# Kernel optimization log

Measured on AMD Instinct MI355X. Metric: run time of the kernel, lower is better.

## Reference

```python
import jax, jax.numpy as jnp
import numpy as np

NIN = 1024
NOUT = 1024
NHEADS = 16
DHEAD = NOUT // NHEADS


def setup_inputs() -> dict:
    key = jax.random.key(0)
    k1, k2, k3, k4 = jax.random.split(key, 4)
    y = jax.random.normal(k1, (2, 2048, NIN), dtype=jnp.float32)
    Wqkv = jax.random.normal(k2, (NIN, 3 * NOUT), dtype=jnp.float32) * (1.0 / np.sqrt(NIN))
    Wff = jax.random.normal(k3, (NOUT, NOUT), dtype=jnp.float32) * (1.0 / np.sqrt(NOUT))
    bff = jax.random.normal(k4, (NOUT,), dtype=jnp.float32) * 0.01
    return {"y": y, "Wqkv": Wqkv, "Wff": Wff, "bff": bff}


def reference(y, Wqkv, Wff, bff):
    b, n, _ = y.shape
    qkv = y @ Wqkv  # [b, n, 3*nout]
    qkv = qkv.reshape(b, n, 3, NHEADS, DHEAD).transpose(2, 0, 3, 1, 4)
    q, k, v = qkv[0], qkv[1], qkv[2]  # each [b, h, n, d]
    att = jnp.einsum('bhqd,bhkd->bhqk', q, k)
    causal = jnp.triu(jnp.ones((n, n), dtype=bool), k=1)
    att = jnp.where(causal, -jnp.inf, att)
    att = jax.nn.softmax(att / jnp.sqrt(jnp.float32(DHEAD)), axis=-1)
    ctx = jnp.einsum('bhqk,bhkd->bhqd', att, v)
    ctx = ctx.transpose(0, 2, 1, 3).reshape(b, n, NOUT)
    return ctx @ Wff + bff
```

## Files before the change

kernel.cpp:

```cpp
#include <hip/hip_runtime.h>
#include <stdint.h>

#define NHEADS 16
#define DHEAD 64
#define SEQ 2048
#define BATCH 2
#define NINF 1024
#define NOUTF 1024
#define N3 3072
#define MTOT 4096

typedef unsigned short US;
typedef __attribute__((ext_vector_type(8))) short short8;
typedef __attribute__((ext_vector_type(4))) short short4v;
typedef __attribute__((ext_vector_type(4))) float f32x4;

__device__ inline US f2bf(float f) {
  union { float f; unsigned u; } v; v.f = f;
  unsigned r = v.u + 0x7fffu + ((v.u >> 16) & 1u);
  return (US)(r >> 16);
}

__device__ inline f32x4 mfma16(short8 a, short8 b, f32x4 c) {
  return __builtin_amdgcn_mfma_f32_16x16x32_bf16(a, b, c, 0, 0, 0);
}

__device__ inline f32x4 mfma16k16(short4v a, short4v b, f32x4 c) {
  return __builtin_amdgcn_mfma_f32_16x16x16bf16_1k(a, b, c, 0, 0, 0);
}

__device__ inline void async16(const US* g, US* l) {
  __builtin_amdgcn_global_load_lds(
      (const __attribute__((address_space(1))) unsigned int*)g,
      (__attribute__((address_space(3))) unsigned int*)l, 16, 0, 0);
}

__global__ void k_convert(const float* __restrict__ src, US* __restrict__ dst, int n4) {
  int i = blockIdx.x * blockDim.x + threadIdx.x;
  if (i >= n4) return;
  float4 v = ((const float4*)src)[i];
  ushort4 o;
  o.x = f2bf(v.x); o.y = f2bf(v.y); o.z = f2bf(v.z); o.w = f2bf(v.w);
  ((ushort4*)dst)[i] = o;
}

__global__ void k_wtrans(const float* __restrict__ Wqkv, const float* __restrict__ Wff,
                         US* __restrict__ dq, US* __restrict__ df) {
  __shared__ float tile[32][33];
  int bxi = blockIdx.x;
  const float* src; US* dst; int C;
  if (bxi < 96) { src = Wqkv; dst = dq; C = N3; }
  else          { src = Wff;  dst = df; C = NOUTF; bxi -= 96; }
  int bx = bxi * 32, by = blockIdx.y * 32;
  int tx = threadIdx.x, ty = threadIdx.y;
  for (int i = 0; i < 32; i += 8)
    tile[ty + i][tx] = src[(size_t)(by + ty + i) * C + bx + tx];
  __syncthreads();
  for (int i = 0; i < 32; i += 8)
    dst[(size_t)(bx + ty + i) * 1024 + by + tx] = f2bf(tile[tx][ty + i]);
}

__global__ __launch_bounds__(256) void k_gemm_qkv(
    const US* __restrict__ A,
    const US* __restrict__ Bt,
    US* __restrict__ qbuf, US* __restrict__ kbuf, US* __restrict__ vtbuf) {
  __shared__ US As[128 * 32];
  __shared__ US Bs[128 * 32];
  int tid = threadIdx.x;
  int wave = tid >> 6, lane = tid & 63, lm = lane & 15, lk = lane >> 4;
  int wm = wave >> 1, wn = wave & 1;
  int mbase = blockIdx.y * 128, nbase = blockIdx.x * 128;
  int which = nbase >> 10;

  f32x4 acc[4][4];
#pragma unroll
  for (int i = 0; i < 4; ++i)
#pragma unroll
    for (int j = 0; j < 4; ++j) acc[i][j] = (f32x4){0.f, 0.f, 0.f, 0.f};

  const US* ga = A + (size_t)(mbase + (tid >> 2)) * NINF + (tid & 3) * 8;
  const US* gb = Bt + (size_t)(nbase + (tid >> 2)) * NINF + (tid & 3) * 8;
  US* la = As + tid * 8;
  US* lb = Bs + tid * 8;

  for (int kt = 0; kt < NINF / 32; ++kt) {
    int ko = kt * 32;
    async16(ga + ko, la);
    async16(ga + ko + (size_t)64 * NINF, la + 64 * 32);
    async16(gb + ko, lb);
    async16(gb + ko + (size_t)64 * NINF, lb + 64 * 32);
    __syncthreads();
    short8 a[4], b[4];
#pragma unroll
    for (int i = 0; i < 4; ++i)
      a[i] = *(const short8*)(As + (wm * 64 + i * 16 + lm) * 32 + lk * 8);
#pragma unroll
    for (int j = 0; j < 4; ++j)
      b[j] = *(const short8*)(Bs + (wn * 64 + j * 16 + lm) * 32 + lk * 8);
    if (which != 2) {
#pragma unroll
      for (int i = 0; i < 4; ++i)
#pragma unroll
        for (int j = 0; j < 4; ++j) acc[i][j] = mfma16(b[j], a[i], acc[i][j]);
    } else {
#pragma unroll
      for (int i = 0; i < 4; ++i)
#pragma unroll
        for (int j = 0; j < 4; ++j) acc[i][j] = mfma16(a[i], b[j], acc[i][j]);
    }
    __syncthreads();
  }

  int hh = ((nbase + wn * 64) & 1023) >> 6;
  if (which != 2) {
    US* dsts = (which == 0) ? qbuf : kbuf;
    float sc = (which == 0) ? 0.18033688011112042f : 1.f;
#pragma unroll
    for (int i = 0; i < 4; ++i) {
      int row = mbase + wm * 64 + i * 16 + lm;
      int bh = (row >> 11) * NHEADS + hh;
      int s = row & (SEQ - 1);
      US* base = dsts + ((size_t)bh * SEQ + s) * DHEAD;
#pragma unroll
      for (int j = 0; j < 4; ++j) {
        int d0 = j * 16 + lk * 4;
        uint32_t lo = (uint32_t)f2bf(acc[i][j][0] * sc) | ((uint32_t)f2bf(acc[i][j][1] * sc) << 16);
        uint32_t hi = (uint32_t)f2bf(acc[i][j][2] * sc) | ((uint32_t)f2bf(acc[i][j][3] * sc) << 16);
        uint2 pv; pv.x = lo; pv.y = hi;
        *(uint2*)(base + d0) = pv;
      }
    }
  } else {
#pragma unroll
    for (int j = 0; j < 4; ++j) {
      int d = j * 16 + lm;
#pragma unroll
      for (int i = 0; i < 4; ++i) {
        int row0 = mbase + wm * 64 + i * 16 + lk * 4;
        int bh = (row0 >> 11) * NHEADS + hh;
        int s0 = row0 & (SEQ - 1);
        uint32_t lo = (uint32_t)f2bf(acc[i][j][0]) | ((uint32_t)f2bf(acc[i][j][1]) << 16);
        uint32_t hi = (uint32_t)f2bf(acc[i][j][2]) | ((uint32_t)f2bf(acc[i][j][3]) << 16);
        uint2 pv; pv.x = lo; pv.y = hi;
        *(uint2*)(vtbuf + ((size_t)bh * DHEAD + d) * SEQ + s0) = pv;
      }
    }
  }
}

__global__ __launch_bounds__(256) void k_attn(
    const US* __restrict__ qbuf, const US* __restrict__ kbuf,
    const US* __restrict__ vtbuf, US* __restrict__ ctx) {
  __shared__ US Ks[2][64 * 64];
  __shared__ US Vs[2][64 * 64];
  int tid = threadIdx.x;
  int w = tid >> 6, lane = tid & 63;
  int lm = lane & 15, lk = lane >> 4;
  int bl = blockIdx.x;
  int xcd = bl & 7, g = bl >> 3;
  int bh = (g & 3) * 8 + xcd;
  int q4 = g >> 2;
  int rnd = q4 >> 3, qq = q4 & 7;
  int s = (rnd == 0) ? 31 - qq : (rnd == 1) ? qq : (rnd == 2) ? 23 - qq : 8 + qq;
  int qb = s * 64 + w * 16;
  int nt = s + 1;

  const US* kbase = kbuf + (size_t)bh * SEQ * DHEAD;
  const US* vtb = vtbuf + (size_t)bh * DHEAD * SEQ;
  const US* qr = qbuf + ((size_t)bh * SEQ + qb + lm) * DHEAD + lk * 8;
  short8 qf0 = *(const short8*)(qr);
  short8 qf1 = *(const short8*)(qr + 32);

  int swz = ((lane & 7) ^ (lane >> 3)) * 8;
  const US* gsrc[4];
  US* ldst[4];
  int step[4];
#pragma unroll
  for (int j = 0; j < 4; ++j) {
    int u = w + 4 * j;
    if (u < 8) {
      gsrc[j] = kbase + (size_t)(u * 8 + (lane >> 3)) * DHEAD + swz;
      ldst[j] = &Ks[0][0] + u * 512 + lane * 8;
      step[j] = 64 * DHEAD;
    } else {
      int i = u - 8;
      gsrc[j] = vtb + (size_t)(i * 8 + (lane >> 3)) * SEQ + swz;
      ldst[j] = &Vs[0][0] + i * 512 + lane * 8;
      step[j] = 64;
    }
  }

  int xorv = lm & 7;
  int ck0 = ((lk) ^ xorv) * 16;
  int ck1 = ((4 + lk) ^ xorv) * 16;
  int cv[4];
#pragma unroll
  for (int kg = 0; kg < 4; ++kg)
    cv[kg] = (((kg * 2 + (lk >> 1)) ^ xorv) * 16) + (lk & 1) * 8;

  f32x4 o[4];
#pragma unroll
  for (int dg = 0; dg < 4; ++dg) o[dg] = (f32x4){0.f, 0.f, 0.f, 0.f};
  f32x4 lacc = (f32x4){0.f, 0.f, 0.f, 0.f};
  const short4v kones = {(short)0x3F80, (short)0x3F80, (short)0x3F80, (short)0x3F80};

  auto body = [&](const char* Kc, const char* Vc, int kg, bool dm) {
    const char* kr = Kc + (kg * 16 + lm) * 128;
    short8 ka0 = *(const short8*)(kr + ck0);
    short8 ka1 = *(const short8*)(kr + ck1);
    f32x4 st = (f32x4){0.f, 0.f, 0.f, 0.f};
    st = mfma16(ka0, qf0, st);
    st = mfma16(ka1, qf1, st);
    uint32_t ue[4];
#pragma unroll
    for (int r = 0; r < 4; ++r) {
      float v = st[r];
      if (dm && (lk * 4 + r > lm)) v = -INFINITY;
      union { float f; uint32_t u; } cv2;
      cv2.f = exp2f(v);
      ue[r] = cv2.u + 0x8000u;
    }
    union { short4v s4; uint32_t u[2]; } pk;
    pk.u[0] = __builtin_amdgcn_perm(ue[1], ue[0], 0x07060302u);
    pk.u[1] = __builtin_amdgcn_perm(ue[3], ue[2], 0x07060302u);
    lacc = mfma16k16(kones, pk.s4, lacc);
    const char* vr = Vc + lm * 128 + cv[kg];
#pragma unroll
    for (int dg = 0; dg < 4; ++dg) {
      short4v va = *(const short4v*)(vr + dg * 2048);
      o[dg] = mfma16k16(va, pk.s4, o[dg]);
    }
  };

#pragma unroll
  for (int j = 0; j < 4; ++j) { async16(gsrc[j], ldst[j]); gsrc[j] += step[j]; }
  if (nt > 1) {
#pragma unroll
    for (int j = 0; j < 4; ++j) { async16(gsrc[j], ldst[j] + 4096); gsrc[j] += step[j]; }
  }

  for (int t = 0; t < nt; ++t) {
    if (t + 1 < nt) asm volatile("s_waitcnt vmcnt(4)" ::: "memory");
    else            asm volatile("s_waitcnt vmcnt(0)" ::: "memory");
    __builtin_amdgcn_s_barrier();
    asm volatile("" ::: "memory");
    const char* Kc = (const char*)Ks + (t & 1) * 8192;
    const char* Vc = (const char*)Vs + (t & 1) * 8192;
    if (t < s) {
#pragma unroll
      for (int kg = 0; kg < 4; ++kg) body(Kc, Vc, kg, false);
    } else {
      for (int kg = 0; kg < w; ++kg) body(Kc, Vc, kg, false);
      body(Kc, Vc, w, true);
    }
    asm volatile("" ::: "memory");
    __builtin_amdgcn_s_barrier();
    asm volatile("" ::: "memory");
    if (t + 2 < nt) {
#pragma unroll
      for (int j = 0; j < 4; ++j) {
        async16(gsrc[j], ldst[j] + (t & 1) * 4096);
        gsrc[j] += step[j];
      }
    }
  }

  float inv = 1.f / lacc[0];

  US* crow = ctx + ((size_t)(bh >> 4) * SEQ + qb + lm) * NOUTF + (bh & 15) * DHEAD;
#pragma unroll
  for (int dg = 0; dg < 4; ++dg) {
    union { short4v s4; uint32_t u[2]; } pk;
    pk.u[0] = (uint32_t)f2bf(o[dg][0] * inv) | ((uint32_t)f2bf(o[dg][1] * inv) << 16);
    pk.u[1] = (uint32_t)f2bf(o[dg][2] * inv) | ((uint32_t)f2bf(o[dg][3] * inv) << 16);
    *(short4v*)(crow + dg * 16 + lk * 4) = pk.s4;
  }
}

__global__ __launch_bounds__(256) void k_gemm_out(
    const US* __restrict__ A, const US* __restrict__ Bt,
    const float* __restrict__ bias, float* __restrict__ out) {
  __shared__ US As[128 * 32];
  __shared__ US Bs[64 * 32];
  int tid = threadIdx.x;
  int wave = tid >> 6, lane = tid & 63, lm = lane & 15, lk = lane >> 4;
  int mbase = blockIdx.y * 128, nbase = blockIdx.x * 64;

  f32x4 acc[2][4];
#pragma unroll
  for (int i = 0; i < 2; ++i)
#pragma unroll
    for (int j = 0; j < 4; ++j) acc[i][j] = (f32x4){0.f, 0.f, 0.f, 0.f};

  const US* ga = A + (size_t)(mbase + (tid >> 2)) * NOUTF + (tid & 3) * 8;
  const US* gb = Bt + (size_t)(nbase + (tid >> 2)) * NOUTF + (tid & 3) * 8;
  US* la = As + tid * 8;
  US* lb = Bs + tid * 8;

  for (int kt = 0; kt < NOUTF / 32; ++kt) {
    int ko = kt * 32;
    async16(ga + ko, la);
    async16(ga + ko + (size_t)64 * NOUTF, la + 64 * 32);
    async16(gb + ko, lb);
    __syncthreads();
    short8 a[2], b[4];
#pragma unroll
    for (int i = 0; i < 2; ++i)
      a[i] = *(const short8*)(As + (wave * 32 + i * 16 + lm) * 32 + lk * 8);
#pragma unroll
    for (int j = 0; j < 4; ++j)
      b[j] = *(const short8*)(Bs + (j * 16 + lm) * 32 + lk * 8);
#pragma unroll
    for (int i = 0; i < 2; ++i)
#pragma unroll
      for (int j = 0; j < 4; ++j) acc[i][j] = mfma16(b[j], a[i], acc[i][j]);
    __syncthreads();
  }

#pragma unroll
  for (int j = 0; j < 4; ++j) {
    int n0 = nbase + j * 16 + lk * 4;
    float4 bv = *(const float4*)(bias + n0);
#pragma unroll
    for (int i = 0; i < 2; ++i) {
      int row = mbase + wave * 32 + i * 16 + lm;
      float4 ov;
      ov.x = acc[i][j][0] + bv.x;
      ov.y = acc[i][j][1] + bv.y;
      ov.z = acc[i][j][2] + bv.z;
      ov.w = acc[i][j][3] + bv.w;
      *(float4*)(out + (size_t)row * NOUTF + n0) = ov;
    }
  }
}

extern "C" void kernel_launch(void* const* d_in, const int* in_sizes, int n_in,
                              void* d_out, int out_size, void* d_ws, size_t ws_size,
                              hipStream_t stream) {
  const float* y    = (const float*)d_in[0];
  const float* Wqkv = (const float*)d_in[1];
  const float* Wff  = (const float*)d_in[2];
  const float* bff  = (const float*)d_in[3];
  float* out = (float*)d_out;

  char* ws = (char*)d_ws;
  US* ybf   = (US*)(ws);
  US* ctx   = (US*)(ws);
  US* wqkvt = (US*)(ws + (8u << 20));
  US* wfft  = (US*)(ws + (14u << 20));
  US* qbuf  = (US*)(ws + (16u << 20));
  US* kbuf  = (US*)(ws + (24u << 20));
  US* vtbuf = (US*)(ws + (40u << 20));

  k_convert<<<MTOT * NINF / 4 / 256, 256, 0, stream>>>(y, ybf, MTOT * NINF / 4);
  k_wtrans<<<dim3(128, 32), dim3(32, 8), 0, stream>>>(Wqkv, Wff, wqkvt, wfft);
  k_gemm_qkv<<<dim3(N3 / 128, MTOT / 128), 256, 0, stream>>>(ybf, wqkvt, qbuf, kbuf, vtbuf);
  k_attn<<<dim3(1024), 256, 0, stream>>>(qbuf, kbuf, vtbuf, ctx);
  k_gemm_out<<<dim3(NOUTF / 64, MTOT / 128), 256, 0, stream>>>(ctx, wfft, bff, out);
}
```

Baseline: 192.9 us.

## Double-buffer LDS tiles in QKV and output GEMMs with async prefetch

Both projection GEMMs now keep two LDS buffers and prefetch the k-tile two steps ahead with async global-to-LDS loads. Explicit vmcnt waits and raw barriers replace the per-iteration __syncthreads. The goal is to overlap global memory latency with MFMA work instead of stalling each k-step. This doubles LDS use per block, which may lower occupancy, and depends on the hand-counted vmcnt values matching the number of outstanding loads.

```diff
diff --git a/kernel.cpp b/kernel.cpp
--- a/kernel.cpp
+++ b/kernel.cpp
@@ -64,8 +64,8 @@
     const US* __restrict__ A,
     const US* __restrict__ Bt,
     US* __restrict__ qbuf, US* __restrict__ kbuf, US* __restrict__ vtbuf) {
-  __shared__ US As[128 * 32];
-  __shared__ US Bs[128 * 32];
+  __shared__ US As[2][128 * 32];
+  __shared__ US Bs[2][128 * 32];
   int tid = threadIdx.x;
   int wave = tid >> 6, lane = tid & 63, lm = lane & 15, lk = lane >> 4;
   int wm = wave >> 1, wn = wave & 1;
@@ -80,35 +80,70 @@
 
   const US* ga = A + (size_t)(mbase + (tid >> 2)) * NINF + (tid & 3) * 8;
   const US* gb = Bt + (size_t)(nbase + (tid >> 2)) * NINF + (tid & 3) * 8;
-  US* la = As + tid * 8;
-  US* lb = Bs + tid * 8;
-
-  for (int kt = 0; kt < NINF / 32; ++kt) {
+  US* la = &As[0][0] + tid * 8;
+  US* lb = &Bs[0][0] + tid * 8;
+
+  auto STAGE = [&](int kt, int buf) {
     int ko = kt * 32;
-    async16(ga + ko, la);
-    async16(ga + ko + (size_t)64 * NINF, la + 64 * 32);
-    async16(gb + ko, lb);
-    async16(gb + ko + (size_t)64 * NINF, lb + 64 * 32);
-    __syncthreads();
-    short8 a[4], b[4];
-#pragma unroll
-    for (int i = 0; i < 4; ++i)
-      a[i] = *(const short8*)(As + (wm * 64 + i * 16 + lm) * 32 + lk * 8);
-#pragma unroll
-    for (int j = 0; j < 4; ++j)
-      b[j] = *(const short8*)(Bs + (wn * 64 + j * 16 + lm) * 32 + lk * 8);
-    if (which != 2) {
+    async16(ga + ko, la + buf * 4096);
+    async16(ga + ko + (size_t)64 * NINF, la + buf * 4096 + 2048);
+    async16(gb + ko, lb + buf * 4096);
+    async16(gb + ko + (size_t)64 * NINF, lb + buf * 4096 + 2048);
+  };
+
+  STAGE(0, 0);
+  STAGE(1, 1);
+
+  if (which != 2) {
+    for (int t = 0; t < 32; ++t) {
+      if (t < 31) asm volatile("s_waitcnt vmcnt(4)" ::: "memory");
+      else        asm volatile("s_waitcnt vmcnt(0)" ::: "memory");
+      __builtin_amdgcn_s_barrier();
+      asm volatile("" ::: "memory");
+      int buf = t & 1;
+      const US* Ab = &As[0][0] + buf * 4096;
+      const US* Bb = &Bs[0][0] + buf * 4096;
+      short8 a[4], b[4];
 #pragma unroll
       for (int i = 0; i < 4; ++i)
+        a[i] = *(const short8*)(Ab + (wm * 64 + i * 16 + lm) * 32 + lk * 8);
+#pragma unroll
+      for (int j = 0; j < 4; ++j)
+        b[j] = *(const short8*)(Bb + (wn * 64 + j * 16 + lm) * 32 + lk * 8);
+#pragma unroll
+      for (int i = 0; i < 4; ++i)
 #pragma unroll
         for (int j = 0; j < 4; ++j) acc[i][j] = mfma16(b[j], a[i], acc[i][j]);
-    } else {
+      asm volatile("" ::: "memory");
+      __builtin_amdgcn_s_barrier();
+      asm volatile("" ::: "memory");
+      if (t + 2 < 32) STAGE(t + 2, buf);
+    }
+  } else {
+    for (int t = 0; t < 32; ++t) {
+      if (t < 31) asm volatile("s_waitcnt vmcnt(4)" ::: "memory");
+      else        asm volatile("s_waitcnt vmcnt(0)" ::: "memory");
+      __builtin_amdgcn_s_barrier();
+      asm volatile("" ::: "memory");
+      int buf = t & 1;
+      const US* Ab = &As[0][0] + buf * 4096;
+      const US* Bb = &Bs[0][0] + buf * 4096;
+      short8 a[4], b[4];
 #pragma unroll
       for (int i = 0; i < 4; ++i)
+        a[i] = *(const short8*)(Ab + (wm * 64 + i * 16 + lm) * 32 + lk * 8);
+#pragma unroll
+      for (int j = 0; j < 4; ++j)
+        b[j] = *(const short8*)(Bb + (wn * 64 + j * 16 + lm) * 32 + lk * 8);
+#pragma unroll
+      for (int i = 0; i < 4; ++i)
 #pragma unroll
         for (int j = 0; j < 4; ++j) acc[i][j] = mfma16(a[i], b[j], acc[i][j]);
-    }
-    __syncthreads();
+      asm volatile("" ::: "memory");
+      __builtin_amdgcn_s_barrier();
+      asm volatile("" ::: "memory");
+      if (t + 2 < 32) STAGE(t + 2, buf);
+    }
   }
 
   int hh = ((nbase + wn * 64) & 1023) >> 6;
@@ -280,8 +315,8 @@
 __global__ __launch_bounds__(256) void k_gemm_out(
     const US* __restrict__ A, const US* __restrict__ Bt,
     const float* __restrict__ bias, float* __restrict__ out) {
-  __shared__ US As[128 * 32];
-  __shared__ US Bs[64 * 32];
+  __shared__ US As[2][128 * 32];
+  __shared__ US Bs[2][64 * 32];
   int tid = threadIdx.x;
   int wave = tid >> 6, lane = tid & 63, lm = lane & 15, lk = lane >> 4;
   int mbase = blockIdx.y * 128, nbase = blockIdx.x * 64;
@@ -294,27 +329,42 @@
 
   const US* ga = A + (size_t)(mbase + (tid >> 2)) * NOUTF + (tid & 3) * 8;
   const US* gb = Bt + (size_t)(nbase + (tid >> 2)) * NOUTF + (tid & 3) * 8;
-  US* la = As + tid * 8;
-  US* lb = Bs + tid * 8;
-
-  for (int kt = 0; kt < NOUTF / 32; ++kt) {
+  US* la = &As[0][0] + tid * 8;
+  US* lb = &Bs[0][0] + tid * 8;
+
+  auto STAGE = [&](int kt, int buf) {
     int ko = kt * 32;
-    async16(ga + ko, la);
-    async16(ga + ko + (size_t)64 * NOUTF, la + 64 * 32);
-    async16(gb + ko, lb);
-    __syncthreads();
+    async16(ga + ko, la + buf * 4096);
+    async16(ga + ko + (size_t)64 * NOUTF, la + buf * 4096 + 2048);
+    async16(gb + ko, lb + buf * 2048);
+  };
+
+  STAGE(0, 0);
+  STAGE(1, 1);
+
+  for (int t = 0; t < 32; ++t) {
+    if (t < 31) asm volatile("s_waitcnt vmcnt(3)" ::: "memory");
+    else        asm volatile("s_waitcnt vmcnt(0)" ::: "memory");
+    __builtin_amdgcn_s_barrier();
+    asm volatile("" ::: "memory");
+    int buf = t & 1;
+    const US* Ab = &As[0][0] + buf * 4096;
+    const US* Bb = &Bs[0][0] + buf * 2048;
     short8 a[2], b[4];
 #pragma unroll
     for (int i = 0; i < 2; ++i)
-      a[i] = *(const short8*)(As + (wave * 32 + i * 16 + lm) * 32 + lk * 8);
+      a[i] = *(const short8*)(Ab + (wave * 32 + i * 16 + lm) * 32 + lk * 8);
 #pragma unroll
     for (int j = 0; j < 4; ++j)
-      b[j] = *(const short8*)(Bs + (j * 16 + lm) * 32 + lk * 8);
+      b[j] = *(const short8*)(Bb + (j * 16 + lm) * 32 + lk * 8);
 #pragma unroll
     for (int i = 0; i < 2; ++i)
 #pragma unroll
       for (int j = 0; j < 4; ++j) acc[i][j] = mfma16(b[j], a[i], acc[i][j]);
-    __syncthreads();
+    asm volatile("" ::: "memory");
+    __builtin_amdgcn_s_barrier();
+    asm volatile("" ::: "memory");
+    if (t + 2 < 32) STAGE(t + 2, buf);
   }
 
 #pragma unroll
```

Measured after the change: 187.0 us. -3.0%, faster.
